# Performance work log

Hardware: AMD Instinct MI355X
Metric: run time of the kernel (lower is better)

Reference implementation:

```python
import jax, jax.numpy as jnp
import numpy as np

# Static config matching init_kwargs
DG = 8          # deformable groups
KH, KW = 3, 3
STRIDE, PAD, DIL = 1, 1, 1


def setup_inputs() -> dict:
    key = jax.random.key(0)
    k1, k2, k3, k4 = jax.random.split(key, 4)
    B, C, H, W = 4, 128, 128, 128
    Cout = 128
    K = KH * KW
    x = jax.random.normal(k1, (B, C, H, W), dtype=jnp.float32)
    offset = jax.random.normal(k2, (B, 2 * DG * K, H, W), dtype=jnp.float32)
    mask = jax.random.uniform(k3, (B, DG * K, H, W), dtype=jnp.float32)
    stdv = 1.0 / np.sqrt(C * KH * KW)
    weight = jax.random.uniform(k4, (Cout, C, KH, KW), dtype=jnp.float32,
                                minval=-stdv, maxval=stdv)
    bias = jnp.zeros((Cout,), dtype=jnp.float32)
    return {"x": x, "offset": offset, "mask": mask, "weight": weight, "bias": bias}


def _deform_conv2d(x, offset, mask, weight, bias):
    B, C, H, W = x.shape
    Cout = weight.shape[0]
    K = KH * KW
    Ho = (H + 2 * PAD - DIL * (KH - 1) - 1) // STRIDE + 1
    Wo = (W + 2 * PAD - DIL * (KW - 1) - 1) // STRIDE + 1
    Cg = C // DG

    # offsets: channel layout [dg, k, (dy, dx)]
    off = offset.reshape(B, DG, K, 2, Ho, Wo)
    dy, dx = off[:, :, :, 0], off[:, :, :, 1]          # [B, DG, K, Ho, Wo]
    m = mask.reshape(B, DG, K, Ho, Wo)

    ky, kx = jnp.meshgrid(jnp.arange(KH), jnp.arange(KW), indexing='ij')
    ky, kx = ky.reshape(K), kx.reshape(K)
    # base sampling grid per kernel tap: [K, Ho] / [K, Wo]
    py = (jnp.arange(Ho) * STRIDE - PAD)[None, :] + (ky * DIL)[:, None]
    px = (jnp.arange(Wo) * STRIDE - PAD)[None, :] + (kx * DIL)[:, None]

    sy = dy + py[None, None, :, :, None].astype(dy.dtype)  # [B, DG, K, Ho, Wo]
    sx = dx + px[None, None, :, None, :].astype(dx.dtype)

    y0f = jnp.floor(sy); x0f = jnp.floor(sx)
    ly = sy - y0f; lx = sx - x0f
    y0 = y0f.astype(jnp.int32); x0 = x0f.astype(jnp.int32)

    x_g = x.reshape(B, DG, Cg, H * W)

    def gather(iy, ix):
        valid = ((iy >= 0) & (iy < H) & (ix >= 0) & (ix < W)).astype(x.dtype)
        idx = jnp.clip(iy, 0, H - 1) * W + jnp.clip(ix, 0, W - 1)
        flat = idx.reshape(B, DG, 1, K * Ho * Wo)
        v = jnp.take_along_axis(x_g, flat, axis=3).reshape(B, DG, Cg, K, Ho, Wo)
        return v * valid[:, :, None]

    w00 = ((1 - ly) * (1 - lx))[:, :, None]
    w01 = ((1 - ly) * lx)[:, :, None]
    w10 = (ly * (1 - lx))[:, :, None]
    w11 = (ly * lx)[:, :, None]

    val = (gather(y0, x0) * w00 + gather(y0, x0 + 1) * w01 +
           gather(y0 + 1, x0) * w10 + gather(y0 + 1, x0 + 1) * w11)
    val = val * m[:, :, None]                         # modulation
    sampled = val.reshape(B, C, K, Ho, Wo)

    w = weight.reshape(Cout, C, K)
    out = jnp.einsum('bckhw,ock->bohw', sampled, w)
    return out + bias[None, :, None, None]


def reference(x, offset, mask, weight, bias):
    return _deform_conv2d(x, offset, mask, weight, bias)
```

## Files before the change

kernel.cpp:

```cpp
#include <hip/hip_runtime.h>
#include <hip/hip_fp16.h>


#define NB    4
#define NC    128
#define NH    128
#define NW    128
#define NCOUT 128
#define NDG   8
#define NCG   16
#define NK    9
#define NCK   1152
#define NHW   16384
#define GK    160
#define ROWP  168
#define WROW  1280

typedef __attribute__((ext_vector_type(4))) float f32x4;
typedef _Float16 half8 __attribute__((ext_vector_type(8)));

union C16 { uint4 u[2]; __half2 h[8]; };

__device__ __forceinline__ unsigned pk2h(float a, float b) {
  return (unsigned)__half_as_ushort(__float2half_rn(a)) |
         ((unsigned)__half_as_ushort(__float2half_rn(b)) << 16);
}

__global__ __launch_bounds__(256)
void prep(const float* __restrict__ x, const float* __restrict__ w,
          ushort* __restrict__ xt, ushort* __restrict__ wf) {
  __shared__ __align__(16) unsigned LDSU[1024 * 9];
  const int tid = threadIdx.x;

  if (blockIdx.x < 128) {
    const int o = blockIdx.x;
    float* WL = (float*)LDSU;
    const float4* src = (const float4*)(w + o * NCK);
    for (int i = tid; i < NCK / 4; i += 256) ((float4*)WL)[i] = src[i];
    __syncthreads();
    unsigned* dst = (unsigned*)wf + o * (WROW / 2);
    for (int t = tid; t < WROW / 2; t += 256) {
      const int g = t / 80, r = t - g * 80;
      unsigned v = 0;
      if (r < 72) {
        const int k = r >> 3;
        const int c = g * NCG + (r & 7) * 2;
        v = pk2h(WL[c * NK + k], WL[(c + 1) * NK + k]);
      }
      dst[t] = v;
    }
  } else {
    const int blk  = blockIdx.x - 128;
    const int slab = blk >> 4;
    const int hw0  = (blk & 15) * 1024;
    const float* xb = x + (size_t)slab * NCG * NHW + hw0;
#pragma unroll
    for (int cp = 0; cp < 8; ++cp) {
#pragma unroll
      for (int i = 0; i < 4; ++i) {
        const int hw = tid + 256 * i;
        LDSU[hw * 9 + cp] =
            pk2h(xb[(2 * cp) * NHW + hw], xb[(2 * cp + 1) * NHW + hw]);
      }
    }
    __syncthreads();
    uint4* dst = (uint4*)(xt + ((size_t)slab * NHW + hw0) * NCG);
#pragma unroll
    for (int j = 0; j < 8; ++j) {
      const int lin = tid + 256 * j;
      const int hw = lin >> 1, q = lin & 1;
      uint4 v;
      v.x = LDSU[hw * 9 + q * 4 + 0];
      v.y = LDSU[hw * 9 + q * 4 + 1];
      v.z = LDSU[hw * 9 + q * 4 + 2];
      v.w = LDSU[hw * 9 + q * 4 + 3];
      dst[lin] = v;
    }
  }
}

__device__ __forceinline__ void sample_one(
    int t, int g, int b, int ho, float dy, float dx, float mm,
    const ushort* __restrict__ xt, ushort* __restrict__ S) {
  const int p  = t & 127;
  const int k  = t >> 7;
  const int ky = k / 3, kx = k - ky * 3;

  const float sy = dy + (float)(ho - 1 + ky);
  const float sx = dx + (float)(p - 1 + kx);
  const float y0f = floorf(sy), x0f = floorf(sx);
  const float ly = sy - y0f, lx = sx - x0f;
  const int y0 = (int)y0f, x0 = (int)x0f;
  const int y1 = y0 + 1,  x1 = x0 + 1;
  const float hy = 1.f - ly, hx = 1.f - lx;

  float w00 = hy * hx * mm, w01 = hy * lx * mm;
  float w10 = ly * hx * mm, w11 = ly * lx * mm;
  if (y0 < 0 || y0 >= NH) { w00 = 0.f; w01 = 0.f; }
  if (y1 < 0 || y1 >= NH) { w10 = 0.f; w11 = 0.f; }
  if (x0 < 0 || x0 >= NW) { w00 = 0.f; w10 = 0.f; }
  if (x1 < 0 || x1 >= NW) { w01 = 0.f; w11 = 0.f; }

  const int yc0 = min(max(y0, 0), NH - 1);
  const int yc1 = min(max(y1, 0), NH - 1);
  const int xc0 = min(max(x0, 0), NW - 1);
  const int xc1 = min(max(x1, 0), NW - 1);

  const ushort* xg = xt + (size_t)(b * NDG + g) * NHW * NCG;
  const uint4* q00 = (const uint4*)(xg + (yc0 * NW + xc0) * NCG);
  const uint4* q01 = (const uint4*)(xg + (yc0 * NW + xc1) * NCG);
  const uint4* q10 = (const uint4*)(xg + (yc1 * NW + xc0) * NCG);
  const uint4* q11 = (const uint4*)(xg + (yc1 * NW + xc1) * NCG);

  C16 v00, v01, v10, v11, r;
  v00.u[0] = q00[0]; v00.u[1] = q00[1];
  v01.u[0] = q01[0]; v01.u[1] = q01[1];
  v10.u[0] = q10[0]; v10.u[1] = q10[1];
  v11.u[0] = q11[0]; v11.u[1] = q11[1];

  const __half2 W00 = __float2half2_rn(w00);
  const __half2 W01 = __float2half2_rn(w01);
  const __half2 W10 = __float2half2_rn(w10);
  const __half2 W11 = __float2half2_rn(w11);
#pragma unroll
  for (int i = 0; i < 8; ++i) {
    __half2 a = __hmul2(v00.h[i], W00);
    a = __hfma2(v01.h[i], W01, a);
    a = __hfma2(v10.h[i], W10, a);
    a = __hfma2(v11.h[i], W11, a);
    r.h[i] = a;
  }
  ushort* dp = &S[p * ROWP + k * 16];
  *(uint4*)dp = r.u[0];
  *((uint4*)dp + 1) = r.u[1];
}

__global__ __launch_bounds__(512, 4)
void dcn_main(const float* __restrict__ off,
              const float* __restrict__ msk,
              const ushort* __restrict__ xt,
              const ushort* __restrict__ wf,
              const float* __restrict__ bias,
              float* __restrict__ out) {
  __shared__ __align__(16) ushort S[128 * ROWP];

  const int tid = threadIdx.x;
  const int blk = blockIdx.x;
  const int b   = blk >> 7;
  const int ho  = blk & 127;

  const int lane = tid & 63;
  const int wv   = tid >> 6;
  const int l15  = lane & 15;
  const int kq   = lane >> 4;

  const float* offB = off + (size_t)b * 144 * NHW + ho * NW;
  const float* mskB = msk + (size_t)b * 72  * NHW + ho * NW;

  for (int i = tid; i < 128 * 8; i += 512) {
    ((unsigned*)S)[(i >> 3) * (ROWP / 2) + 72 + (i & 7)] = 0;
  }
  __syncthreads();

  f32x4 acc[8];
#pragma unroll
  for (int m = 0; m < 8; ++m) acc[m] = {0.f, 0.f, 0.f, 0.f};

  const int t0 = tid;
  const int t1 = tid + 512;
  const int t2 = tid + 1024;
  const int p0 = t0 & 127, k0 = t0 >> 7;
  const int p1 = t1 & 127, k1 = t1 >> 7;
  const int p2 = t2 & 127, k2 = t2 >> 7;

  for (int g = 0; g < 8; ++g) {
    if (g) __syncthreads();

    const int gk0 = g * 9 + k0, gk1 = g * 9 + k1, gk2 = g * 9 + k2;
    const float dy0 = offB[(gk0 * 2) * NHW + p0];
    const float dx0 = offB[(gk0 * 2 + 1) * NHW + p0];
    const float m0  = mskB[gk0 * NHW + p0];
    const float dy1 = offB[(gk1 * 2) * NHW + p1];
    const float dx1 = offB[(gk1 * 2 + 1) * NHW + p1];
    const float m1  = mskB[gk1 * NHW + p1];
    float dy2 = 0.f, dx2 = 0.f, m2 = 0.f;
    if (tid < 128) {
      dy2 = offB[(gk2 * 2) * NHW + p2];
      dx2 = offB[(gk2 * 2 + 1) * NHW + p2];
      m2  = mskB[gk2 * NHW + p2];
    }
    sample_one(t0, g, b, ho, dy0, dx0, m0, xt, S);
    sample_one(t1, g, b, ho, dy1, dx1, m1, xt, S);
    if (tid < 128) sample_one(t2, g, b, ho, dy2, dx2, m2, xt, S);
    __syncthreads();

    const ushort* bw = wf + (size_t)(wv * 16 + l15) * WROW + g * GK + kq * 8;
    const ushort* sa = &S[l15 * ROWP + kq * 8];
#pragma unroll
    for (int ks = 0; ks < 5; ++ks) {
      const half8 bfrag = *(const half8*)(bw + ks * 32);
#pragma unroll
      for (int m = 0; m < 8; ++m) {
        const half8 a = *(const half8*)(sa + m * 16 * ROWP + ks * 32);
        acc[m] = __builtin_amdgcn_mfma_f32_16x16x32_f16(a, bfrag, acc[m], 0, 0, 0);
      }
    }
  }

  const int c0 = wv * 16 + l15;
  const float bs = bias[c0];
  float* op = out + (size_t)(b * NCOUT + c0) * NHW + ho * NW + kq * 4;
#pragma unroll
  for (int m = 0; m < 8; ++m) {
    float4 r = {acc[m][0] + bs, acc[m][1] + bs, acc[m][2] + bs, acc[m][3] + bs};
    *(float4*)(op + m * 16) = r;
  }
}

extern "C" void kernel_launch(void* const* d_in, const int* in_sizes, int n_in,
                              void* d_out, int out_size, void* d_ws, size_t ws_size,
                              hipStream_t stream) {
  const float* x    = (const float*)d_in[0];
  const float* off  = (const float*)d_in[1];
  const float* msk  = (const float*)d_in[2];
  const float* wgt  = (const float*)d_in[3];
  const float* bias = (const float*)d_in[4];
  float* out = (float*)d_out;

  ushort* xt = (ushort*)d_ws;
  ushort* wf = xt + (size_t)NB * NDG * NHW * NCG;

  hipLaunchKernelGGL(prep, dim3(640), dim3(256), 0, stream, x, wgt, xt, wf);
  hipLaunchKernelGGL(dcn_main, dim3(512), dim3(512), 0, stream,
                     off, msk, xt, wf, bias, out);
}
```

Measured before the change: 188.4 us.

## Split output rows into half-width tiles with 256-thread blocks and prefetch offsets

```diff
diff --git a/kernel.cpp b/kernel.cpp
--- a/kernel.cpp
+++ b/kernel.cpp
@@ -80,14 +80,13 @@
 }
 
 __device__ __forceinline__ void sample_one(
-    int t, int g, int b, int ho, float dy, float dx, float mm,
+    int p, int k, int g, int b, int ho, int wo0,
+    float dy, float dx, float mm,
     const ushort* __restrict__ xt, ushort* __restrict__ S) {
-  const int p  = t & 127;
-  const int k  = t >> 7;
   const int ky = k / 3, kx = k - ky * 3;
 
   const float sy = dy + (float)(ho - 1 + ky);
-  const float sx = dx + (float)(p - 1 + kx);
+  const float sx = dx + (float)(wo0 + p - 1 + kx);
   const float y0f = floorf(sy), x0f = floorf(sx);
   const float ly = sy - y0f, lx = sx - x0f;
   const int y0 = (int)y0f, x0 = (int)x0f;
@@ -135,85 +134,112 @@
   *((uint4*)dp + 1) = r.u[1];
 }
 
-__global__ __launch_bounds__(512, 4)
+__global__ __launch_bounds__(256, 4)
 void dcn_main(const float* __restrict__ off,
               const float* __restrict__ msk,
               const ushort* __restrict__ xt,
               const ushort* __restrict__ wf,
               const float* __restrict__ bias,
               float* __restrict__ out) {
-  __shared__ __align__(16) ushort S[128 * ROWP];
-
-  const int tid = threadIdx.x;
-  const int blk = blockIdx.x;
-  const int b   = blk >> 7;
-  const int ho  = blk & 127;
+  __shared__ __align__(16) ushort S[64 * ROWP];
+
+  const int tid  = threadIdx.x;
+  const int blk0 = blockIdx.x;
+  const int blk  = (blk0 & 7) * 128 + (blk0 >> 3);
+  const int b    = blk >> 8;
+  const int ho   = (blk >> 1) & 127;
+  const int wo0  = (blk & 1) * 64;
 
   const int lane = tid & 63;
   const int wv   = tid >> 6;
   const int l15  = lane & 15;
   const int kq   = lane >> 4;
 
-  const float* offB = off + (size_t)b * 144 * NHW + ho * NW;
-  const float* mskB = msk + (size_t)b * 72  * NHW + ho * NW;
-
-  for (int i = tid; i < 128 * 8; i += 512) {
+  const float* offB = off + (size_t)b * 144 * NHW + ho * NW + wo0;
+  const float* mskB = msk + (size_t)b * 72  * NHW + ho * NW + wo0;
+
+  for (int i = tid; i < 64 * 8; i += 256) {
     ((unsigned*)S)[(i >> 3) * (ROWP / 2) + 72 + (i & 7)] = 0;
   }
-  __syncthreads();
-
-  f32x4 acc[8];
-#pragma unroll
-  for (int m = 0; m < 8; ++m) acc[m] = {0.f, 0.f, 0.f, 0.f};
-
-  const int t0 = tid;
-  const int t1 = tid + 512;
-  const int t2 = tid + 1024;
-  const int p0 = t0 & 127, k0 = t0 >> 7;
-  const int p1 = t1 & 127, k1 = t1 >> 7;
-  const int p2 = t2 & 127, k2 = t2 >> 7;
+
+  f32x4 acc[4][2];
+#pragma unroll
+  for (int m = 0; m < 4; ++m) {
+    acc[m][0] = {0.f, 0.f, 0.f, 0.f};
+    acc[m][1] = {0.f, 0.f, 0.f, 0.f};
+  }
+
+  const int p0 = tid & 63;
+  const int k0 = tid >> 6;
+  const int k1 = k0 + 4;
+
+  float dy0, dx0, mm0, dy1, dx1, mm1, dy2 = 0.f, dx2 = 0.f, mm2 = 0.f;
+  {
+    const int gka = k0, gkb = k1;
+    dy0 = offB[(gka * 2) * NHW + p0];
+    dx0 = offB[(gka * 2 + 1) * NHW + p0];
+    mm0 = mskB[gka * NHW + p0];
+    dy1 = offB[(gkb * 2) * NHW + p0];
+    dx1 = offB[(gkb * 2 + 1) * NHW + p0];
+    mm1 = mskB[gkb * NHW + p0];
+    if (tid < 64) {
+      dy2 = offB[16 * NHW + p0];
+      dx2 = offB[17 * NHW + p0];
+      mm2 = mskB[8 * NHW + p0];
+    }
+  }
 
   for (int g = 0; g < 8; ++g) {
     if (g) __syncthreads();
 
-    const int gk0 = g * 9 + k0, gk1 = g * 9 + k1, gk2 = g * 9 + k2;
-    const float dy0 = offB[(gk0 * 2) * NHW + p0];
-    const float dx0 = offB[(gk0 * 2 + 1) * NHW + p0];
-    const float m0  = mskB[gk0 * NHW + p0];
-    const float dy1 = offB[(gk1 * 2) * NHW + p1];
-    const float dx1 = offB[(gk1 * 2 + 1) * NHW + p1];
-    const float m1  = mskB[gk1 * NHW + p1];
-    float dy2 = 0.f, dx2 = 0.f, m2 = 0.f;
-    if (tid < 128) {
-      dy2 = offB[(gk2 * 2) * NHW + p2];
-      dx2 = offB[(gk2 * 2 + 1) * NHW + p2];
-      m2  = mskB[gk2 * NHW + p2];
-    }
-    sample_one(t0, g, b, ho, dy0, dx0, m0, xt, S);
-    sample_one(t1, g, b, ho, dy1, dx1, m1, xt, S);
-    if (tid < 128) sample_one(t2, g, b, ho, dy2, dx2, m2, xt, S);
+    sample_one(p0, k0, g, b, ho, wo0, dy0, dx0, mm0, xt, S);
+    sample_one(p0, k1, g, b, ho, wo0, dy1, dx1, mm1, xt, S);
+    if (tid < 64) sample_one(p0, 8, g, b, ho, wo0, dy2, dx2, mm2, xt, S);
+
+    if (g < 7) {
+      const int gka = (g + 1) * 9 + k0, gkb = (g + 1) * 9 + k1;
+      dy0 = offB[(gka * 2) * NHW + p0];
+      dx0 = offB[(gka * 2 + 1) * NHW + p0];
+      mm0 = mskB[gka * NHW + p0];
+      dy1 = offB[(gkb * 2) * NHW + p0];
+      dx1 = offB[(gkb * 2 + 1) * NHW + p0];
+      mm1 = mskB[gkb * NHW + p0];
+      if (tid < 64) {
+        const int gkc = (g + 1) * 9 + 8;
+        dy2 = offB[(gkc * 2) * NHW + p0];
+        dx2 = offB[(gkc * 2 + 1) * NHW + p0];
+        mm2 = mskB[gkc * NHW + p0];
+      }
+    }
     __syncthreads();
 
-    const ushort* bw = wf + (size_t)(wv * 16 + l15) * WROW + g * GK + kq * 8;
-    const ushort* sa = &S[l15 * ROWP + kq * 8];
+    const ushort* bw0 = wf + (size_t)(wv * 32 + l15) * WROW + g * GK + kq * 8;
+    const ushort* bw1 = bw0 + 16 * WROW;
+    const ushort* sa  = &S[l15 * ROWP + kq * 8];
 #pragma unroll
     for (int ks = 0; ks < 5; ++ks) {
-      const half8 bfrag = *(const half8*)(bw + ks * 32);
-#pragma unroll
-      for (int m = 0; m < 8; ++m) {
+      const half8 bf0 = *(const half8*)(bw0 + ks * 32);
+      const half8 bf1 = *(const half8*)(bw1 + ks * 32);
+#pragma unroll
+      for (int m = 0; m < 4; ++m) {
         const half8 a = *(const half8*)(sa + m * 16 * ROWP + ks * 32);
-        acc[m] = __builtin_amdgcn_mfma_f32_16x16x32_f16(a, bfrag, acc[m], 0, 0, 0);
-      }
-    }
-  }
-
-  const int c0 = wv * 16 + l15;
-  const float bs = bias[c0];
-  float* op = out + (size_t)(b * NCOUT + c0) * NHW + ho * NW + kq * 4;
-#pragma unroll
-  for (int m = 0; m < 8; ++m) {
-    float4 r = {acc[m][0] + bs, acc[m][1] + bs, acc[m][2] + bs, acc[m][3] + bs};
-    *(float4*)(op + m * 16) = r;
+        acc[m][0] = __builtin_amdgcn_mfma_f32_16x16x32_f16(a, bf0, acc[m][0], 0, 0, 0);
+        acc[m][1] = __builtin_amdgcn_mfma_f32_16x16x32_f16(a, bf1, acc[m][1], 0, 0, 0);
+      }
+    }
+  }
+
+#pragma unroll
+  for (int j = 0; j < 2; ++j) {
+    const int c0 = wv * 32 + j * 16 + l15;
+    const float bs = bias[c0];
+    float* op = out + (size_t)(b * NCOUT + c0) * NHW + ho * NW + wo0 + kq * 4;
+#pragma unroll
+    for (int m = 0; m < 4; ++m) {
+      float4 r = {acc[m][j][0] + bs, acc[m][j][1] + bs,
+                  acc[m][j][2] + bs, acc[m][j][3] + bs};
+      *(float4*)(op + m * 16) = r;
+    }
   }
 }
 
@@ -231,6 +257,6 @@
   ushort* wf = xt + (size_t)NB * NDG * NHW * NCG;
 
   hipLaunchKernelGGL(prep, dim3(640), dim3(256), 0, stream, x, wgt, xt, wf);
-  hipLaunchKernelGGL(dcn_main, dim3(512), dim3(512), 0, stream,
+  hipLaunchKernelGGL(dcn_main, dim3(1024), dim3(256), 0, stream,
                      off, msk, xt, wf, bias, out);
 }
```

After: 209.3 us. +11.1%, slower.
